# Kernel optimization log

Measured on AMD Instinct MI355X. Metric: run time of the kernel, lower is better.

Reference implementation:

```python
import jax, jax.numpy as jnp
import numpy as np

N_HEADS = 16


def setup_inputs() -> dict:
    key = jax.random.key(0)
    ks = jax.random.split(key, 5)
    B, T, C = 4, 2048, 1024
    x = jax.random.normal(ks[0], (B, T, C), dtype=jnp.float32)
    w_qkv = jax.random.normal(ks[1], (C, 3 * C), dtype=jnp.float32) * (1.0 / np.sqrt(C))
    b_qkv = jnp.zeros((3 * C,), dtype=jnp.float32)
    w_proj = jax.random.normal(ks[2], (C, C), dtype=jnp.float32) * (1.0 / np.sqrt(C))
    b_proj = jnp.zeros((C,), dtype=jnp.float32)
    return {"x": x, "w_qkv": w_qkv, "b_qkv": b_qkv, "w_proj": w_proj, "b_proj": b_proj}


def reference(x, w_qkv, b_qkv, w_proj, b_proj):
    B, T, C = x.shape
    H = N_HEADS
    D = C // H
    scale = 1.0 / np.sqrt(D).astype(np.float32)
    qkv = x @ w_qkv + b_qkv                      # [B,T,3C]
    qkv = qkv.reshape(B, T, 3, H, D)
    q, k, v = [jnp.transpose(qkv[:, :, i], (0, 2, 1, 3)) for i in range(3)]  # [B,H,T,D]
    attn = jnp.einsum('bhqd,bhkd->bhqk', q, k) * scale
    causal = jnp.tril(jnp.ones((T, T), dtype=bool))
    attn = jnp.where(causal[None, None], attn, -jnp.inf)
    attn = jax.nn.softmax(attn, axis=-1)
    out = jnp.einsum('bhqk,bhkd->bhqd', attn, v)  # [B,H,T,D]
    out = jnp.transpose(out, (0, 2, 1, 3)).reshape(B, T, C)
    return out @ w_proj + b_proj
```

## Files before the change

### kernel.cpp

```cpp
#include <hip/hip_runtime.h>
#include <cstdint>

typedef unsigned short u16;
typedef uint32_t u32;
typedef __attribute__((ext_vector_type(8))) short bf16x8;
typedef __attribute__((ext_vector_type(4))) short bf16x4;
typedef __attribute__((ext_vector_type(4))) float f32x4;

#define NB 4
#define NT 2048
#define NC 1024
#define NH 16
#define ND 64
#define NM (NB*NT)
#define N3C (3*NC)
#define NQT (NT/64)

#define QSCALE 0.18033688011112042f

static __device__ __forceinline__ u16 f2bf(float f){
  union { float f; uint32_t u; } v; v.f = f;
  return (u16)((v.u + 0x7fffu + ((v.u >> 16) & 1u)) >> 16);
}

static __device__ __forceinline__ void gld_lds16(void* lds, const void* g){
  auto lp = reinterpret_cast<__attribute__((address_space(3))) uint32_t*>(
      reinterpret_cast<uintptr_t>(lds));
  auto gp = reinterpret_cast<__attribute__((address_space(1))) uint32_t*>(
      reinterpret_cast<uintptr_t>(g));
  __builtin_amdgcn_global_load_lds(gp, lp, 16, 0, 0);
}

static __device__ __forceinline__ f32x4 mfma16(bf16x4 a, bf16x4 b, f32x4 c){
#if __has_builtin(__builtin_amdgcn_mfma_f32_16x16x16bf16_1k)
  return __builtin_amdgcn_mfma_f32_16x16x16bf16_1k(a, b, c, 0, 0, 0);
#else
  asm("v_mfma_f32_16x16x16_bf16 %0, %1, %2, %0" : "+v"(c) : "v"(a), "v"(b));
  return c;
#endif
}

__global__ __launch_bounds__(256) void k_cast(const float* __restrict__ in,
                                              u16* __restrict__ out){
  const int i = (blockIdx.x * 256 + threadIdx.x) * 4;
  const float4 vv = *reinterpret_cast<const float4*>(in + i);
  union { u16 s[4]; uint64_t u; } pk;
  pk.s[0] = f2bf(vv.x); pk.s[1] = f2bf(vv.y);
  pk.s[2] = f2bf(vv.z); pk.s[3] = f2bf(vv.w);
  *reinterpret_cast<uint64_t*>(out + i) = pk.u;
}

__global__ __launch_bounds__(256) void k_transpose_cast(const float* __restrict__ in,
                                                        u16* __restrict__ out,
                                                        int R, int Cc){
  __shared__ float tile[32][33];
  const int bx = blockIdx.x * 32, by = blockIdx.y * 32;
  const int tx = threadIdx.x, ty = threadIdx.y;
#pragma unroll
  for (int i = 0; i < 32; i += 8)
    tile[ty + i][tx] = in[(size_t)(by + ty + i) * Cc + bx + tx];
  __syncthreads();
#pragma unroll
  for (int i = 0; i < 32; i += 8)
    out[(size_t)(bx + ty + i) * R + by + tx] = f2bf(tile[tx][ty + i]);
}

static __device__ __forceinline__ void gemm_mainloop(
    const u16* __restrict__ A, const u16* __restrict__ Bt, int K,
    int m0, int n0, u16* As, u16* Bs, f32x4 acc[4][4])
{
  const int tid = threadIdx.x;
  const int wave = tid >> 6, lane = tid & 63;
  const int wm = wave >> 1, wn = wave & 1;
  const int o0 = tid * 8, o1 = o0 + 2048;
  const u16* Ag0 = A  + (size_t)(m0 + (o0 >> 5)) * K + (o0 & 31);
  const u16* Ag1 = A  + (size_t)(m0 + (o1 >> 5)) * K + (o1 & 31);
  const u16* Bg0 = Bt + (size_t)(n0 + (o0 >> 5)) * K + (o0 & 31);
  const u16* Bg1 = Bt + (size_t)(n0 + (o1 >> 5)) * K + (o1 & 31);
  u16* AsW = As + wave * 512;
  u16* BsW = Bs + wave * 512;
  const int kb = (lane >> 4) * 8, rl = lane & 15;

  for (int kt = 0; kt < K; kt += 32){
    gld_lds16(AsW,        Ag0 + kt);
    gld_lds16(AsW + 2048, Ag1 + kt);
    gld_lds16(BsW,        Bg0 + kt);
    gld_lds16(BsW + 2048, Bg1 + kt);
    __syncthreads();
    bf16x8 af[4], bfr[4];
#pragma unroll
    for (int i = 0; i < 4; i++){
      af[i]  = *reinterpret_cast<const bf16x8*>(&As[(wm * 64 + i * 16 + rl) * 32 + kb]);
      bfr[i] = *reinterpret_cast<const bf16x8*>(&Bs[(wn * 64 + i * 16 + rl) * 32 + kb]);
    }
#pragma unroll
    for (int i = 0; i < 4; i++)
#pragma unroll
      for (int j = 0; j < 4; j++)
        acc[i][j] = __builtin_amdgcn_mfma_f32_16x16x32_bf16(af[i], bfr[j], acc[i][j], 0, 0, 0);
    __syncthreads();
  }
}

__global__ __launch_bounds__(256) void k_gemm_qkv(
    const u16* __restrict__ A, const u16* __restrict__ Bt,
    const float* __restrict__ bias,
    u16* __restrict__ qo, u16* __restrict__ ko, u16* __restrict__ vo)
{
  __shared__ u16 As[128 * 32], Bs[128 * 32];
  f32x4 acc[4][4] = {};
  const int m0 = blockIdx.y * 128, n0 = blockIdx.x * 128;
  gemm_mainloop(A, Bt, NC, m0, n0, As, Bs, acc);

  const int tid = threadIdx.x;
  const int wave = tid >> 6, lane = tid & 63;
  const int wm = wave >> 1, wn = wave & 1;
  const int rl = lane & 15, rg = lane >> 4;
  const int which = n0 >> 10;
  if (which == 2){
#pragma unroll
    for (int j = 0; j < 4; j++){
      const int n = n0 + wn * 64 + j * 16 + rl;
      const int cc = n & 1023;
      const int h = cc >> 6, d = cc & 63;
      const float bb = bias[n];
#pragma unroll
      for (int i = 0; i < 4; i++){
        const int mb = m0 + wm * 64 + i * 16 + rg * 4;
        const int b = mb >> 11, t0 = mb & 2047;
        const size_t bhb = ((size_t)(b * NH + h)) * NT * ND;
        union { u16 s[4]; uint64_t u; } pk4;
#pragma unroll
        for (int r = 0; r < 4; r++) pk4.s[r] = f2bf(acc[i][j][r] + bb);
        *reinterpret_cast<uint64_t*>(
          &vo[bhb + (size_t)(t0 >> 6) * 4096 + d * 64 + ((((t0 >> 2) & 15) ^ (d & 7)) << 2)]) = pk4.u;
      }
    }
  } else {
#pragma unroll
    for (int j = 0; j < 4; j++){
      const int n = n0 + wn * 64 + j * 16 + rl;
      const int cc = n & 1023;
      const int h = cc >> 6, d = cc & 63;
      const float bb = bias[n];
#pragma unroll
      for (int i = 0; i < 4; i++){
#pragma unroll
        for (int r = 0; r < 4; r++){
          const int m = m0 + wm * 64 + i * 16 + rg * 4 + r;
          const int b = m >> 11, t = m & 2047;
          const size_t bhb = ((size_t)(b * NH + h)) * NT * ND;
          const float val = acc[i][j][r] + bb;
          if (which == 0){
            qo[bhb + (size_t)t * ND + d] = f2bf(val * QSCALE);
          } else {
            ko[bhb + (size_t)(t >> 6) * 4096 + (t & 63) * 64 + (d ^ ((t & 7) << 3))] = f2bf(val);
          }
        }
      }
    }
  }
}

__global__ __launch_bounds__(256) void k_gemm_proj(
    const u16* __restrict__ A, const u16* __restrict__ Bt,
    const float* __restrict__ bias, float* __restrict__ out)
{
  __shared__ u16 As[128 * 32], Bs[128 * 32];
  f32x4 acc[4][4] = {};
  const int m0 = blockIdx.y * 128, n0 = blockIdx.x * 128;
  gemm_mainloop(A, Bt, NC, m0, n0, As, Bs, acc);

  const int tid = threadIdx.x;
  const int wave = tid >> 6, lane = tid & 63;
  const int wm = wave >> 1, wn = wave & 1;
  const int rl = lane & 15, rg = lane >> 4;
#pragma unroll
  for (int i = 0; i < 4; i++){
#pragma unroll
    for (int r = 0; r < 4; r++){
      const int m = m0 + wm * 64 + i * 16 + rg * 4 + r;
#pragma unroll
      for (int j = 0; j < 4; j++){
        const int n = n0 + wn * 64 + j * 16 + rl;
        out[(size_t)m * NC + n] = acc[i][j][r] + bias[n];
      }
    }
  }
}

static __device__ __forceinline__ void qkt(const u16* __restrict__ KsC,
                                           bf16x8 qf0, bf16x8 qf1,
                                           int cl, int g, f32x4 s[4])
{
  __builtin_amdgcn_s_setprio(1);
#pragma unroll
  for (int nf = 0; nf < 4; nf++){
    const int kj = nf * 16 + cl;
    const u16* krow = &KsC[kj * 64];
    const bf16x8 kf0 = *reinterpret_cast<const bf16x8*>(&krow[((0 + g) ^ (kj & 7)) * 8]);
    const bf16x8 kf1 = *reinterpret_cast<const bf16x8*>(&krow[((4 + g) ^ (kj & 7)) * 8]);
    f32x4 a = {};
    a = __builtin_amdgcn_mfma_f32_16x16x32_bf16(kf0, qf0, a, 0, 0, 0);
    a = __builtin_amdgcn_mfma_f32_16x16x32_bf16(kf1, qf1, a, 0, 0, 0);
    s[nf] = a;
  }
  __builtin_amdgcn_s_setprio(0);
}

static __device__ __forceinline__ void maskdiag(f32x4 s[4], int wave, int cl, int g){
  const int qrl = wave * 16 + cl;
#pragma unroll
  for (int nf = 0; nf < 4; nf++)
#pragma unroll
    for (int r = 0; r < 4; r++)
      if (nf * 16 + g * 4 + r > qrl) s[nf][r] = -3e38f;
}

static __device__ __forceinline__ void sm_pv(
    f32x4 s[4], f32x4 o[4], float& mrun, float& lrun,
    const u16* __restrict__ VtC, int cl, int g)
{
  float rmax = -3e38f;
#pragma unroll
  for (int nf = 0; nf < 4; nf++)
#pragma unroll
    for (int r = 0; r < 4; r++) rmax = fmaxf(rmax, s[nf][r]);
  rmax = fmaxf(rmax, __shfl_xor(rmax, 16));
  rmax = fmaxf(rmax, __shfl_xor(rmax, 32));
  if (!__all(rmax <= mrun + 8.0f)){
    const float mnew = fmaxf(mrun, rmax);
    const float alpha = exp2f(mrun - mnew);
    mrun = mnew;
    lrun *= alpha;
    const float a0 = __shfl(alpha, g * 4 + 0);
    const float a1 = __shfl(alpha, g * 4 + 1);
    const float a2 = __shfl(alpha, g * 4 + 2);
    const float a3 = __shfl(alpha, g * 4 + 3);
#pragma unroll
    for (int fo = 0; fo < 4; fo++){
      o[fo][0] *= a0; o[fo][1] *= a1; o[fo][2] *= a2; o[fo][3] *= a3;
    }
  }
  float rs = 0.f;
#pragma unroll
  for (int nf = 0; nf < 4; nf++)
#pragma unroll
    for (int r = 0; r < 4; r++){
      s[nf][r] = exp2f(s[nf][r] - mrun);
      rs += s[nf][r];
    }
  rs += __shfl_xor(rs, 16);
  rs += __shfl_xor(rs, 32);
  lrun += rs;

  u32 pk[4][2];
#pragma unroll
  for (int nf = 0; nf < 4; nf++){
    asm("v_cvt_pk_bf16_f32 %0, %1, %2" : "=v"(pk[nf][0]) : "v"(s[nf][0]), "v"(s[nf][1]));
    asm("v_cvt_pk_bf16_f32 %0, %1, %2" : "=v"(pk[nf][1]) : "v"(s[nf][2]), "v"(s[nf][3]));
  }
  __builtin_amdgcn_s_setprio(1);
#pragma unroll
  for (int nf = 0; nf < 4; nf++){
    union { u32 u[2]; bf16x4 v; } pa;
    pa.u[0] = pk[nf][0]; pa.u[1] = pk[nf][1];
#pragma unroll
    for (int fo = 0; fo < 4; fo++){
      const int d = fo * 16 + cl;
      const bf16x4 vf = *reinterpret_cast<const bf16x4*>(
          &VtC[d * 64 + (((nf * 4 + g) ^ (d & 7)) << 2)]);
      o[fo] = mfma16(pa.v, vf, o[fo]);
    }
  }
  __builtin_amdgcn_s_setprio(0);
}

__global__ __launch_bounds__(256) void k_flash(
    const u16* __restrict__ q, const u16* __restrict__ k,
    const u16* __restrict__ v, u16* __restrict__ ao)
{
  __shared__ u16 Ks[2][4096];
  __shared__ u16 Vt[2][4096];
  const int tid = threadIdx.x, wave = tid >> 6, lane = tid & 63;
  const int cl = lane & 15, g = lane >> 4;
  const int c0 = wave * 2;
  const int px = blockIdx.x, bh = blockIdx.y;
  const int qt1 = px, qt2 = NQT - 1 - px;
  const int ntot = qt2 + 1;
  const size_t base = (size_t)bh * NT * ND;
  const u16* kg0 = k + base;
  const u16* vg0 = v + base;

  bf16x8 q1f0, q1f1, q2f0, q2f1;
  {
    const u16* qr1 = q + base + (size_t)(qt1 * 64 + wave * 16 + cl) * ND;
    q1f0 = *reinterpret_cast<const bf16x8*>(qr1 + g * 8);
    q1f1 = *reinterpret_cast<const bf16x8*>(qr1 + 32 + g * 8);
    const u16* qr2 = q + base + (size_t)(qt2 * 64 + wave * 16 + cl) * ND;
    q2f0 = *reinterpret_cast<const bf16x8*>(qr2 + g * 8);
    q2f1 = *reinterpret_cast<const bf16x8*>(qr2 + 32 + g * 8);
  }
  asm volatile("" : "+v"(q1f0), "+v"(q1f1), "+v"(q2f0), "+v"(q2f1));

  f32x4 o1[4] = {}, o2[4] = {};
  float m1 = -1e30f, l1 = 0.f, m2 = -1e30f, l2 = 0.f;

  gld_lds16(&Ks[0][(c0    ) * 512], kg0 + (c0    ) * 512 + lane * 8);
  gld_lds16(&Ks[0][(c0 + 1) * 512], kg0 + (c0 + 1) * 512 + lane * 8);
  gld_lds16(&Vt[0][(c0    ) * 512], vg0 + (c0    ) * 512 + lane * 8);
  gld_lds16(&Vt[0][(c0 + 1) * 512], vg0 + (c0 + 1) * 512 + lane * 8);

  for (int t = 0; t < ntot; ++t){
    const int cur = t & 1, nxt = cur ^ 1;
    if (t + 1 < ntot){
      const u16* kg = kg0 + (size_t)(t + 1) * 4096;
      const u16* vg = vg0 + (size_t)(t + 1) * 4096;
      gld_lds16(&Ks[nxt][(c0    ) * 512], kg + (c0    ) * 512 + lane * 8);
      gld_lds16(&Ks[nxt][(c0 + 1) * 512], kg + (c0 + 1) * 512 + lane * 8);
      gld_lds16(&Vt[nxt][(c0    ) * 512], vg + (c0    ) * 512 + lane * 8);
      gld_lds16(&Vt[nxt][(c0 + 1) * 512], vg + (c0 + 1) * 512 + lane * 8);
      asm volatile("s_waitcnt vmcnt(4)" ::: "memory");
    } else {
      asm volatile("s_waitcnt vmcnt(0)" ::: "memory");
    }
    __builtin_amdgcn_sched_barrier(0);
    __builtin_amdgcn_s_barrier();

    const u16* KsC = Ks[cur];
    const u16* VtC = Vt[cur];

    {
      f32x4 s[4];
      qkt(KsC, q2f0, q2f1, cl, g, s);
      if (t == qt2) maskdiag(s, wave, cl, g);
      sm_pv(s, o2, m2, l2, VtC, cl, g);
    }
    if (t <= qt1){
      f32x4 s[4];
      qkt(KsC, q1f0, q1f1, cl, g, s);
      if (t == qt1) maskdiag(s, wave, cl, g);
      sm_pv(s, o1, m1, l1, VtC, cl, g);
    }

    asm volatile("s_waitcnt lgkmcnt(0)" ::: "memory");
    __builtin_amdgcn_sched_barrier(0);
    __builtin_amdgcn_s_barrier();
  }

  float li1[4], li2[4];
#pragma unroll
  for (int r = 0; r < 4; r++){
    li1[r] = 1.0f / __shfl(l1, g * 4 + r);
    li2[r] = 1.0f / __shfl(l2, g * 4 + r);
  }
  const int b = bh >> 4, h = bh & 15;
#pragma unroll
  for (int fo = 0; fo < 4; fo++){
#pragma unroll
    for (int r = 0; r < 4; r++){
      const int c = h * 64 + fo * 16 + cl;
      const int t1 = qt1 * 64 + wave * 16 + g * 4 + r;
      ao[((size_t)b * NT + t1) * NC + c] = f2bf(o1[fo][r] * li1[r]);
      const int t2 = qt2 * 64 + wave * 16 + g * 4 + r;
      ao[((size_t)b * NT + t2) * NC + c] = f2bf(o2[fo][r] * li2[r]);
    }
  }
}

extern "C" void kernel_launch(void* const* d_in, const int* in_sizes, int n_in,
                              void* d_out, int out_size, void* d_ws, size_t ws_size,
                              hipStream_t stream){
  const float* x      = (const float*)d_in[0];
  const float* w_qkv  = (const float*)d_in[1];
  const float* b_qkv  = (const float*)d_in[2];
  const float* w_proj = (const float*)d_in[3];
  const float* b_proj = (const float*)d_in[4];
  float* out = (float*)d_out;

  u16* ws = (u16*)d_ws;
  u16* xb     = ws;
  u16* qb     = ws + 8388608;
  u16* kb     = ws + 16777216;
  u16* vb     = ws + 25165824;
  u16* aob    = ws + 33554432;
  u16* wqkvT  = ws + 41943040;
  u16* wprojT = ws + 45088768;

  k_cast<<<8388608 / 1024, 256, 0, stream>>>(x, xb);
  k_transpose_cast<<<dim3(N3C / 32, NC / 32), dim3(32, 8), 0, stream>>>(w_qkv, wqkvT, NC, N3C);
  k_transpose_cast<<<dim3(NC / 32, NC / 32), dim3(32, 8), 0, stream>>>(w_proj, wprojT, NC, NC);
  k_gemm_qkv<<<dim3(N3C / 128, NM / 128), 256, 0, stream>>>(xb, wqkvT, b_qkv, qb, kb, vb);
  k_flash<<<dim3(NQT / 2, NB * NH), 256, 0, stream>>>(qb, kb, vb, aob);
  k_gemm_proj<<<dim3(NC / 128, NM / 128), 256, 0, stream>>>(aob, wprojT, b_proj, out);
}
```

Measured before the change: 223.2 us.

## Fuse the two query-tile passes in flash attention to share K/V fragment loads

While both paired query tiles are active, each K fragment read from LDS now feeds the QK^T MFMAs for both tiles, and each V fragment feeds both PV MFMAs. This roughly halves LDS fragment reads in that phase and interleaves independent MFMA chains to hide latency. Softmax is split into a helper, and its max and sum reductions become balanced trees, which shortens dependency chains. In exchange, register pressure rises because two score sets and two packed P sets are live at once, which could hurt occupancy or cause spills.

```diff
diff --git a/kernel.cpp b/kernel.cpp
--- a/kernel.cpp
+++ b/kernel.cpp
@@ -217,15 +217,14 @@
       if (nf * 16 + g * 4 + r > qrl) s[nf][r] = -3e38f;
 }
 
-static __device__ __forceinline__ void sm_pv(
-    f32x4 s[4], f32x4 o[4], float& mrun, float& lrun,
-    const u16* __restrict__ VtC, int cl, int g)
-{
-  float rmax = -3e38f;
-#pragma unroll
-  for (int nf = 0; nf < 4; nf++)
-#pragma unroll
-    for (int r = 0; r < 4; r++) rmax = fmaxf(rmax, s[nf][r]);
+static __device__ __forceinline__ void softmax_pk(
+    f32x4 s[4], f32x4 o[4], float& mrun, float& lrun, int g, u32 pk[8])
+{
+  const float t0 = fmaxf(fmaxf(s[0][0], s[0][1]), fmaxf(s[0][2], s[0][3]));
+  const float t1 = fmaxf(fmaxf(s[1][0], s[1][1]), fmaxf(s[1][2], s[1][3]));
+  const float t2 = fmaxf(fmaxf(s[2][0], s[2][1]), fmaxf(s[2][2], s[2][3]));
+  const float t3 = fmaxf(fmaxf(s[3][0], s[3][1]), fmaxf(s[3][2], s[3][3]));
+  float rmax = fmaxf(fmaxf(t0, t1), fmaxf(t2, t3));
   rmax = fmaxf(rmax, __shfl_xor(rmax, 16));
   rmax = fmaxf(rmax, __shfl_xor(rmax, 32));
   if (!__all(rmax <= mrun + 8.0f)){
@@ -242,34 +241,42 @@
       o[fo][0] *= a0; o[fo][1] *= a1; o[fo][2] *= a2; o[fo][3] *= a3;
     }
   }
-  float rs = 0.f;
 #pragma unroll
   for (int nf = 0; nf < 4; nf++)
 #pragma unroll
-    for (int r = 0; r < 4; r++){
+    for (int r = 0; r < 4; r++)
       s[nf][r] = exp2f(s[nf][r] - mrun);
-      rs += s[nf][r];
-    }
+  const float u0 = (s[0][0] + s[0][1]) + (s[0][2] + s[0][3]);
+  const float u1 = (s[1][0] + s[1][1]) + (s[1][2] + s[1][3]);
+  const float u2 = (s[2][0] + s[2][1]) + (s[2][2] + s[2][3]);
+  const float u3 = (s[3][0] + s[3][1]) + (s[3][2] + s[3][3]);
+  float rs = (u0 + u1) + (u2 + u3);
   rs += __shfl_xor(rs, 16);
   rs += __shfl_xor(rs, 32);
   lrun += rs;
-
-  u32 pk[4][2];
 #pragma unroll
   for (int nf = 0; nf < 4; nf++){
-    asm("v_cvt_pk_bf16_f32 %0, %1, %2" : "=v"(pk[nf][0]) : "v"(s[nf][0]), "v"(s[nf][1]));
-    asm("v_cvt_pk_bf16_f32 %0, %1, %2" : "=v"(pk[nf][1]) : "v"(s[nf][2]), "v"(s[nf][3]));
-  }
+    asm("v_cvt_pk_bf16_f32 %0, %1, %2" : "=v"(pk[2*nf  ]) : "v"(s[nf][0]), "v"(s[nf][1]));
+    asm("v_cvt_pk_bf16_f32 %0, %1, %2" : "=v"(pk[2*nf+1]) : "v"(s[nf][2]), "v"(s[nf][3]));
+  }
+}
+
+static __device__ __forceinline__ void sm_pv(
+    f32x4 s[4], f32x4 o[4], float& mrun, float& lrun,
+    const u16* __restrict__ VtC, int cl, int g)
+{
+  u32 pk[8];
+  softmax_pk(s, o, mrun, lrun, g, pk);
   __builtin_amdgcn_s_setprio(1);
 #pragma unroll
-  for (int nf = 0; nf < 4; nf++){
-    union { u32 u[2]; bf16x4 v; } pa;
-    pa.u[0] = pk[nf][0]; pa.u[1] = pk[nf][1];
-#pragma unroll
-    for (int fo = 0; fo < 4; fo++){
-      const int d = fo * 16 + cl;
+  for (int fo = 0; fo < 4; fo++){
+    const int d = fo * 16 + cl;
+#pragma unroll
+    for (int nf = 0; nf < 4; nf++){
       const bf16x4 vf = *reinterpret_cast<const bf16x4*>(
           &VtC[d * 64 + (((nf * 4 + g) ^ (d & 7)) << 2)]);
+      union { u32 u[2]; bf16x4 v; } pa;
+      pa.u[0] = pk[2*nf]; pa.u[1] = pk[2*nf+1];
       o[fo] = mfma16(pa.v, vf, o[fo]);
     }
   }
@@ -330,17 +337,50 @@
     const u16* KsC = Ks[cur];
     const u16* VtC = Vt[cur];
 
-    {
+    if (t <= qt1){
+      f32x4 s1[4], s2[4];
+      __builtin_amdgcn_s_setprio(1);
+#pragma unroll
+      for (int nf = 0; nf < 4; nf++){
+        const int kj = nf * 16 + cl;
+        const u16* krow = &KsC[kj * 64];
+        const bf16x8 kf0 = *reinterpret_cast<const bf16x8*>(&krow[((0 + g) ^ (kj & 7)) * 8]);
+        const bf16x8 kf1 = *reinterpret_cast<const bf16x8*>(&krow[((4 + g) ^ (kj & 7)) * 8]);
+        f32x4 a = {};
+        a = __builtin_amdgcn_mfma_f32_16x16x32_bf16(kf0, q2f0, a, 0, 0, 0);
+        a = __builtin_amdgcn_mfma_f32_16x16x32_bf16(kf1, q2f1, a, 0, 0, 0);
+        s2[nf] = a;
+        f32x4 b = {};
+        b = __builtin_amdgcn_mfma_f32_16x16x32_bf16(kf0, q1f0, b, 0, 0, 0);
+        b = __builtin_amdgcn_mfma_f32_16x16x32_bf16(kf1, q1f1, b, 0, 0, 0);
+        s1[nf] = b;
+      }
+      __builtin_amdgcn_s_setprio(0);
+      if (t == qt1) maskdiag(s1, wave, cl, g);
+      u32 pk2[8], pk1[8];
+      softmax_pk(s2, o2, m2, l2, g, pk2);
+      softmax_pk(s1, o1, m1, l1, g, pk1);
+      __builtin_amdgcn_s_setprio(1);
+#pragma unroll
+      for (int fo = 0; fo < 4; fo++){
+        const int d = fo * 16 + cl;
+#pragma unroll
+        for (int nf = 0; nf < 4; nf++){
+          const bf16x4 vf = *reinterpret_cast<const bf16x4*>(
+              &VtC[d * 64 + (((nf * 4 + g) ^ (d & 7)) << 2)]);
+          union { u32 u[2]; bf16x4 v; } pa2, pa1;
+          pa2.u[0] = pk2[2*nf]; pa2.u[1] = pk2[2*nf+1];
+          pa1.u[0] = pk1[2*nf]; pa1.u[1] = pk1[2*nf+1];
+          o2[fo] = mfma16(pa2.v, vf, o2[fo]);
+          o1[fo] = mfma16(pa1.v, vf, o1[fo]);
+        }
+      }
+      __builtin_amdgcn_s_setprio(0);
+    } else {
       f32x4 s[4];
       qkt(KsC, q2f0, q2f1, cl, g, s);
       if (t == qt2) maskdiag(s, wave, cl, g);
       sm_pv(s, o2, m2, l2, VtC, cl, g);
-    }
-    if (t <= qt1){
-      f32x4 s[4];
-      qkt(KsC, q1f0, q1f1, cl, g, s);
-      if (t == qt1) maskdiag(s, wave, cl, g);
-      sm_pv(s, o1, m1, l1, VtC, cl, g);
     }
 
     asm volatile("s_waitcnt lgkmcnt(0)" ::: "memory");
```

After: 234.6 us. +5.1%, slower.
